# Kernel tuning notes

Measured on AMD Instinct MI355X. Metric: run time of the kernel, lower is better.

The kernel has to match this reference:

```python
import jax, jax.numpy as jnp
import numpy as np

DIM = 2048
NUM_HEADS = 16
NUM_KV_HEADS = 4
HEAD_DIM = DIM // NUM_HEADS  # 128
GROUP = NUM_HEADS // NUM_KV_HEADS  # queries per kv head
B, N = 2, 2048


def setup_inputs() -> dict:
    key = jax.random.key(0)
    ks = jax.random.split(key, 5)
    s = 1.0 / np.sqrt(DIM)
    return {
        "x": jax.random.normal(ks[0], (B, N, DIM), dtype=jnp.float32),
        "Wq": jax.random.normal(ks[1], (DIM, DIM), dtype=jnp.float32) * s,
        "Wk": jax.random.normal(ks[2], (DIM, NUM_KV_HEADS * HEAD_DIM), dtype=jnp.float32) * s,
        "Wv": jax.random.normal(ks[3], (DIM, NUM_KV_HEADS * HEAD_DIM), dtype=jnp.float32) * s,
        "Wo": jax.random.normal(ks[4], (DIM, DIM), dtype=jnp.float32) * s,
    }


def reference(x, Wq, Wk, Wv, Wo):
    Bc, Nc, C = x.shape
    scale = HEAD_DIM ** -0.5
    # projections -> [B, H, N, D] / [B, Hkv, N, D]
    q = (x @ Wq).reshape(Bc, Nc, NUM_HEADS, HEAD_DIM).transpose(0, 2, 1, 3)
    k = (x @ Wk).reshape(Bc, Nc, NUM_KV_HEADS, HEAD_DIM).transpose(0, 2, 1, 3)
    v = (x @ Wv).reshape(Bc, Nc, NUM_KV_HEADS, HEAD_DIM).transpose(0, 2, 1, 3)
    # repeat_interleave over head dim: kv head i serves query heads [i*G, (i+1)*G)
    k = jnp.repeat(k, GROUP, axis=1)  # [B, H, N, D]
    v = jnp.repeat(v, GROUP, axis=1)
    attn = jnp.einsum("bhqd,bhkd->bhqk", q, k) * scale
    attn = jax.nn.softmax(attn, axis=-1)
    out = jnp.einsum("bhqk,bhkd->bhqd", attn, v)  # [B, H, N, D]
    out = out.transpose(0, 2, 1, 3).reshape(Bc, Nc, C)
    return out @ Wo
```

## Files before the change

### kernel.cpp

```cpp
#include <hip/hip_runtime.h>
#include <hip/hip_bf16.h>
#include <cstdint>
#include <cstddef>

typedef __bf16 bf16;
typedef __attribute__((ext_vector_type(8))) __bf16 bf16x8;
typedef __attribute__((ext_vector_type(4))) float f32x4;
typedef __attribute__((ext_vector_type(16))) float f32x16;
typedef unsigned int u32;
typedef __attribute__((ext_vector_type(2))) unsigned int u32x2;

#define DEVINL __device__ __forceinline__

#define QPRESCALE 0.12751741530470082f

DEVINL void gload16(const void* g, void* l) {
  __builtin_amdgcn_global_load_lds(
      (const __attribute__((address_space(1))) void*)g,
      (__attribute__((address_space(3))) void*)l, 16, 0, 0);
}

DEVINL f32x4 mfma16(bf16x8 a, bf16x8 b, f32x4 c) {
  return __builtin_amdgcn_mfma_f32_16x16x32_bf16(a, b, c, 0, 0, 0);
}
DEVINL f32x16 mfma32(bf16x8 a, bf16x8 b, f32x16 c) {
  return __builtin_amdgcn_mfma_f32_32x32x16_bf16(a, b, c, 0, 0, 0);
}
DEVINL u32 cvtpk(float lo, float hi) {
  u32 r;
  asm("v_cvt_pk_bf16_f32 %0, %1, %2" : "=v"(r) : "v"(lo), "v"(hi));
  return r;
}
DEVINL void plswap(u32& a, u32& b) {
  asm("v_permlane32_swap_b32 %0, %1" : "+v"(a), "+v"(b));
}

__global__ __launch_bounds__(256) void prep_kernel(const float* __restrict__ x,
                                                   const float* __restrict__ Wq,
                                                   const float* __restrict__ Wk,
                                                   const float* __restrict__ Wv,
                                                   const float* __restrict__ Wo,
                                                   bf16* __restrict__ xbf,
                                                   bf16* __restrict__ WqkvT,
                                                   bf16* __restrict__ WoT) {
  const int bid = blockIdx.x, t = threadIdx.x;
  if (bid < 4096) {
    int i = bid * 256 + t;
    f32x4 a = ((const f32x4*)x)[2 * i];
    f32x4 b2 = ((const f32x4*)x)[2 * i + 1];
    bf16x8 v;
#pragma unroll
    for (int k = 0; k < 4; ++k) { v[k] = (bf16)a[k]; v[4 + k] = (bf16)b2[k]; }
    ((bf16x8*)xbf)[i] = v;
    return;
  }
  __shared__ float tile[64][65];
  const float* src;
  bf16* dst;
  int N, blk;
  if (bid < 5120)      { src = Wq; dst = WqkvT;                        N = 2048; blk = bid - 4096; }
  else if (bid < 5376) { src = Wk; dst = WqkvT + (size_t)2048 * 2048;  N = 512;  blk = bid - 5120; }
  else if (bid < 5632) { src = Wv; dst = WqkvT + (size_t)2560 * 2048;  N = 512;  blk = bid - 5376; }
  else                 { src = Wo; dst = WoT;                          N = 2048; blk = bid - 5632; }
  const int K = 2048;
  int nt = N >> 6;
  int n0 = (blk % nt) << 6;
  int k0 = (blk / nt) << 6;
  int c = t & 63, rb = t >> 6;
#pragma unroll
  for (int rr = 0; rr < 16; ++rr) {
    int row = rr * 4 + rb;
    tile[row][c] = src[(size_t)(k0 + row) * N + n0 + c];
  }
  __syncthreads();
#pragma unroll
  for (int rr = 0; rr < 16; ++rr) {
    int nrow = rr * 4 + rb;
    dst[(size_t)(n0 + nrow) * K + k0 + c] = (bf16)tile[c][nrow];
  }
}

template <int EPI>
__global__ __launch_bounds__(256) void gemm_bt_kernel(const bf16* __restrict__ A,
                                                      const bf16* __restrict__ BT,
                                                      float* __restrict__ Cout,
                                                      int Mtiles,
                                                      bf16* __restrict__ qb,
                                                      bf16* __restrict__ kb_,
                                                      bf16* __restrict__ vtb) {
  __shared__ __align__(16) unsigned char smem[32768];
  const int t = threadIdx.x, w = t >> 6, lane = t & 63;
  const int l4 = lane >> 4, l16 = lane & 15;
  const int bm = blockIdx.x % Mtiles, bn = blockIdx.x / Mtiles;
  const int wm = w >> 1, wn = w & 1;

  const char* aP[2];
  const char* bP[2];
#pragma unroll
  for (int p = 0; p < 2; ++p) {
    int g = p * 256 + t;
    aP[p] = (const char*)A + (size_t)(bm * 128 + (g >> 2)) * 4096 + (g & 3) * 16;
    bP[p] = (const char*)BT + (size_t)(bn * 128 + (g >> 2)) * 4096 + (g & 3) * 16;
  }
  const unsigned ldsW = w * 1024;

  auto STAGE = [&](unsigned buf, int k0) {
    gload16(aP[0] + k0, smem + buf * 16384 + ldsW);
    gload16(aP[1] + k0, smem + buf * 16384 + 4096 + ldsW);
    gload16(bP[0] + k0, smem + buf * 16384 + 8192 + ldsW);
    gload16(bP[1] + k0, smem + buf * 16384 + 12288 + ldsW);
  };

  const f32x4 fz = {0.f, 0.f, 0.f, 0.f};
  f32x4 acc[4][4];
#pragma unroll
  for (int i = 0; i < 4; ++i)
#pragma unroll
    for (int j = 0; j < 4; ++j) acc[i][j] = fz;

  const int arow = 64 * wm + l16, brow = 64 * wn + l16, kbyte = 16 * l4;

  STAGE(0, 0);
  __syncthreads();

#pragma unroll 2
  for (int tt = 0; tt < 64; ++tt) {
    const unsigned buf = tt & 1;
    if (tt < 63) STAGE(buf ^ 1u, (tt + 1) * 64);
    bf16x8 af[4], bfr[4];
#pragma unroll
    for (int i = 0; i < 4; ++i)
      af[i] = *(const bf16x8*)(smem + buf * 16384 + (arow + 16 * i) * 64 + kbyte);
#pragma unroll
    for (int j = 0; j < 4; ++j)
      bfr[j] = *(const bf16x8*)(smem + buf * 16384 + 8192 + (brow + 16 * j) * 64 + kbyte);
#pragma unroll
    for (int i = 0; i < 4; ++i)
#pragma unroll
      for (int j = 0; j < 4; ++j)
        acc[i][j] = mfma16(af[i], bfr[j], acc[i][j]);
    __syncthreads();
  }

  const int r0 = bm * 128 + 64 * wm + 4 * l4;
  if (EPI == 1) {
#pragma unroll
    for (int j = 0; j < 4; ++j) {
      int col = bn * 128 + 64 * wn + 16 * j + l16;
#pragma unroll
      for (int i = 0; i < 4; ++i)
#pragma unroll
        for (int r = 0; r < 4; ++r)
          Cout[(size_t)(r0 + 16 * i + r) * 2048 + col] = acc[i][j][r];
    }
  } else {
    const int bq = bm >> 4;
#pragma unroll
    for (int j = 0; j < 4; ++j) {
      int col = bn * 128 + 64 * wn + 16 * j + l16;
      if (bn < 16) {
        int hh = col >> 7, d = col & 127;
        bf16* dst = qb + (size_t)((bq * 16 + hh) * 2048) * 128 + d;
#pragma unroll
        for (int i = 0; i < 4; ++i)
#pragma unroll
          for (int r = 0; r < 4; ++r) {
            int n = (r0 + 16 * i + r) & 2047;
            dst[(size_t)n * 128] = (bf16)(acc[i][j][r] * QPRESCALE);
          }
      } else if (bn < 20) {
        int kv = (col >> 7) - 16, d = col & 127;
        bf16* dst = kb_ + (size_t)((bq * 4 + kv) * 2048) * 128 + d;
#pragma unroll
        for (int i = 0; i < 4; ++i)
#pragma unroll
          for (int r = 0; r < 4; ++r) {
            int n = (r0 + 16 * i + r) & 2047;
            dst[(size_t)n * 128] = (bf16)acc[i][j][r];
          }
      } else {
        int kv = (col >> 7) - 20, d = col & 127;
        bf16* dst = vtb + ((size_t)(bq * 4 + kv) * 128 + d) * 2048;
#pragma unroll
        for (int i = 0; i < 4; ++i)
#pragma unroll
          for (int r = 0; r < 4; ++r) {
            int n = (r0 + 16 * i + r) & 2047;
            dst[n] = (bf16)acc[i][j][r];
          }
      }
    }
  }
}

__global__ __launch_bounds__(256, 2) void attn_kernel(const bf16* __restrict__ Q,
                                                      const bf16* __restrict__ K,
                                                      const bf16* __restrict__ VT,
                                                      bf16* __restrict__ AO) {
  __shared__ __align__(16) unsigned char smem[65536];
  const int t = threadIdx.x, w = t >> 6, lane = t & 63;
  const int q = lane & 31, hi = lane >> 5;
  const int pair = blockIdx.x >> 4;
  const int q00 = (blockIdx.x & 15) * 128 + w * 32;
  const int b = pair >> 4, h = pair & 15, kvh = h >> 2;

  bf16x8 qf[8];
  {
    const char* qbase = (const char*)Q +
        ((size_t)((b * 16 + h) * 2048 + q00 + q) * 128 + 8 * hi) * 2;
#pragma unroll
    for (int dk = 0; dk < 8; ++dk) qf[dk] = *(const bf16x8*)(qbase + dk * 32);
  }

  f32x16 acc[4];
#pragma unroll
  for (int dt = 0; dt < 4; ++dt)
#pragma unroll
    for (int r = 0; r < 16; ++r) acc[dt][r] = 0.0f;
  float lacc[16];
#pragma unroll
  for (int r = 0; r < 16; ++r) lacc[r] = 0.0f;

  const char* Kg = (const char*)K + (size_t)((b * 4 + kvh) * 2048) * 256;
  const char* Vg = (const char*)VT + (size_t)((b * 4 + kvh) * 128) * 4096;

  auto STAGE_K = [&](int itn) {
    const unsigned base = (unsigned)(itn & 1) * 16384u;
    const int kb = itn * 64;
#pragma unroll
    for (int p = 0; p < 4; ++p) {
      int g = p * 256 + t;
      int row = g >> 4, cb = (g & 15) * 16;
      gload16(Kg + (size_t)(kb + row) * 256 + (cb ^ ((row & 15) << 4)),
              smem + base + p * 4096 + w * 1024);
    }
  };
  auto STAGE_V = [&](int itn) {
    const unsigned base = 32768u + (unsigned)(itn & 1) * 16384u;
    const int kb = itn * 64;
#pragma unroll
    for (int p = 0; p < 4; ++p) {
      int g = p * 256 + t;
      int row = g >> 3, cb = (g & 7) * 16;
      gload16(Vg + (size_t)row * 4096 + kb * 2 + (cb ^ ((row & 7) << 4)),
              smem + base + p * 4096 + w * 1024);
    }
  };

  auto SMFMA = [&](int itn, f32x16& s0, f32x16& s1) {
    const unsigned base = (unsigned)(itn & 1) * 16384u;
    const unsigned swq = (q & 15) << 4;
#pragma unroll
    for (int r = 0; r < 16; ++r) { s0[r] = 0.0f; s1[r] = 0.0f; }
    __builtin_amdgcn_s_setprio(1);
#pragma unroll
    for (int dk = 0; dk < 8; ++dk) {
      const int cb = dk * 32 + 16 * hi;
      bf16x8 k0 = *(const bf16x8*)(smem + base + q * 256 + (cb ^ swq));
      bf16x8 k1 = *(const bf16x8*)(smem + base + (q + 32) * 256 + (cb ^ swq));
      s0 = mfma32(k0, qf[dk], s0);
      s1 = mfma32(k1, qf[dk], s1);
    }
    __builtin_amdgcn_s_setprio(0);
  };

  auto SOFTMAX = [&](f32x16& s0, f32x16& s1, bf16x8* pa) {
    float p0[16], p1[16];
#pragma unroll
    for (int r = 0; r < 16; ++r) {
      p0[r] = __builtin_amdgcn_exp2f(s0[r]);
      p1[r] = __builtin_amdgcn_exp2f(s1[r]);
    }
#pragma unroll
    for (int r = 0; r < 16; ++r) lacc[r] += p0[r] + p1[r];
#pragma unroll
    for (int ks = 0; ks < 4; ++ks) {
      const int bs = (ks & 1) * 8;
      float* P = (ks >> 1) ? p1 : p0;
      u32 A0 = cvtpk(P[bs + 0], P[bs + 1]);
      u32 A1 = cvtpk(P[bs + 2], P[bs + 3]);
      u32 B0 = cvtpk(P[bs + 4], P[bs + 5]);
      u32 B1 = cvtpk(P[bs + 6], P[bs + 7]);
      plswap(A0, B0);
      plswap(A1, B1);
      union { u32 u[4]; bf16x8 v; } pu;
      pu.u[0] = A0; pu.u[1] = A1; pu.u[2] = B0; pu.u[3] = B1;
      pa[ks] = pu.v;
    }
  };

  auto FUSED = [&](int itn, f32x16& sP0, f32x16& sP1, f32x16& sN0, f32x16& sN1) {
    bf16x8 pa[4];
    SOFTMAX(sP0, sP1, pa);
    const unsigned kbase = (unsigned)(itn & 1) * 16384u;
    const unsigned vbase = 32768u + (unsigned)((itn - 1) & 1) * 16384u;
    const unsigned swq = (q & 15) << 4;
    const unsigned swd = (q & 7) << 4;
#pragma unroll
    for (int r = 0; r < 16; ++r) { sN0[r] = 0.0f; sN1[r] = 0.0f; }
    __builtin_amdgcn_s_setprio(1);
#pragma unroll
    for (int step = 0; step < 8; ++step) {
      const int cb = step * 32 + 16 * hi;
      bf16x8 k0 = *(const bf16x8*)(smem + kbase + q * 256 + (cb ^ swq));
      bf16x8 k1 = *(const bf16x8*)(smem + kbase + (q + 32) * 256 + (cb ^ swq));
      const int ks = step >> 1, dt0 = (step & 1) * 2, dt1 = dt0 + 1;
      const int kcol = ks * 32 + 16 * hi;
      bf16x8 va0 = *(const bf16x8*)(smem + vbase + (dt0 * 32 + q) * 128 + (kcol ^ swd));
      bf16x8 va1 = *(const bf16x8*)(smem + vbase + (dt1 * 32 + q) * 128 + (kcol ^ swd));
      sN0 = mfma32(k0, qf[step], sN0);
      acc[dt0] = mfma32(va0, pa[ks], acc[dt0]);
      sN1 = mfma32(k1, qf[step], sN1);
      acc[dt1] = mfma32(va1, pa[ks], acc[dt1]);
    }
    __builtin_amdgcn_s_setprio(0);
  };

  auto FINLAST = [&](int itn, f32x16& sP0, f32x16& sP1) {
    bf16x8 pa[4];
    SOFTMAX(sP0, sP1, pa);
    const unsigned vbase = 32768u + (unsigned)(itn & 1) * 16384u;
    const unsigned swd = (q & 7) << 4;
    __builtin_amdgcn_s_setprio(1);
#pragma unroll
    for (int ks = 0; ks < 4; ++ks) {
      const int kcol = ks * 32 + 16 * hi;
      bf16x8 va0 = *(const bf16x8*)(smem + vbase + (0 * 32 + q) * 128 + (kcol ^ swd));
      bf16x8 va1 = *(const bf16x8*)(smem + vbase + (1 * 32 + q) * 128 + (kcol ^ swd));
      bf16x8 va2 = *(const bf16x8*)(smem + vbase + (2 * 32 + q) * 128 + (kcol ^ swd));
      bf16x8 va3 = *(const bf16x8*)(smem + vbase + (3 * 32 + q) * 128 + (kcol ^ swd));
      acc[0] = mfma32(va0, pa[ks], acc[0]);
      acc[1] = mfma32(va1, pa[ks], acc[1]);
      acc[2] = mfma32(va2, pa[ks], acc[2]);
      acc[3] = mfma32(va3, pa[ks], acc[3]);
    }
    __builtin_amdgcn_s_setprio(0);
  };

  f32x16 sA0, sA1, sB0, sB1;
  STAGE_K(0);
  __syncthreads();

  STAGE_K(1);
  STAGE_V(0);
  SMFMA(0, sA0, sA1);
  __syncthreads();

#pragma unroll 1
  for (int i = 1; i < 31; i += 2) {
    STAGE_K(i + 1);
    STAGE_V(i);
    FUSED(i, sA0, sA1, sB0, sB1);
    __syncthreads();
    STAGE_K(i + 2);
    STAGE_V(i + 1);
    FUSED(i + 1, sB0, sB1, sA0, sA1);
    __syncthreads();
  }

  STAGE_V(31);
  FUSED(31, sA0, sA1, sB0, sB1);
  __syncthreads();
  FINLAST(31, sB0, sB1);

  float tl[16];
#pragma unroll
  for (int r = 0; r < 16; ++r) tl[r] = lacc[r];
#pragma unroll
  for (int st = 8; st; st >>= 1)
#pragma unroll
    for (int r = 0; r < 8; ++r)
      if (r < st) tl[r] += tl[r + st];
  float l0 = tl[0];
  l0 += __shfl_xor(l0, 32, 64);
  const float inv = 1.0f / l0;
  bf16* aorow = AO + (size_t)(b * 2048 + q00 + q) * 2048 + h * 128;
#pragma unroll
  for (int dt = 0; dt < 4; ++dt)
#pragma unroll
    for (int rq = 0; rq < 4; ++rq) {
      u32 w0 = cvtpk(acc[dt][rq * 4 + 0] * inv, acc[dt][rq * 4 + 1] * inv);
      u32 w1 = cvtpk(acc[dt][rq * 4 + 2] * inv, acc[dt][rq * 4 + 3] * inv);
      u32x2 pr; pr.x = w0; pr.y = w1;
      *(u32x2*)(aorow + dt * 32 + rq * 8 + 4 * hi) = pr;
    }
}

extern "C" void kernel_launch(void* const* d_in, const int* in_sizes, int n_in,
                              void* d_out, int out_size, void* d_ws, size_t ws_size,
                              hipStream_t stream) {
  const float* x = (const float*)d_in[0];
  const float* Wq = (const float*)d_in[1];
  const float* Wk = (const float*)d_in[2];
  const float* Wv = (const float*)d_in[3];
  const float* Wo = (const float*)d_in[4];

  char* ws = (char*)d_ws;
  bf16* xbf = (bf16*)(ws);
  bf16* WqkvT = (bf16*)(ws + 16777216);
  bf16* WoT = (bf16*)(ws + 29360128);
  bf16* Qbuf = (bf16*)(ws + 37748736);
  bf16* Kbuf = (bf16*)(ws + 54525952);
  bf16* VTbuf = (bf16*)(ws + 58720256);

  prep_kernel<<<6656, 256, 0, stream>>>(x, Wq, Wk, Wv, Wo, xbf, WqkvT, WoT);
  gemm_bt_kernel<0><<<768, 256, 0, stream>>>(xbf, WqkvT, nullptr, 32, Qbuf, Kbuf, VTbuf);
  attn_kernel<<<512, 256, 0, stream>>>(Qbuf, Kbuf, VTbuf, xbf);
  gemm_bt_kernel<1><<<512, 256, 0, stream>>>(xbf, WoT, (float*)d_out, 32, nullptr, nullptr, nullptr);
}
```

Baseline: 195.0 us.

## Process 64 query rows per wave in attention to reuse K/V fragments

Each wave now handles two 32-row query tiles instead of one, so every K and V fragment read from LDS feeds two MFMAs. The attention grid is halved to 256 blocks and launch bounds drop to one block per CU. This cuts LDS read traffic and K/V global staging per query. In exchange it roughly doubles register pressure (accumulators, scores, Q fragments) and lowers occupancy. With 256 blocks on a 256-CU part, each CU may get only one block, leaving little latency hiding.

```diff
diff --git a/kernel.cpp b/kernel.cpp
--- a/kernel.cpp
+++ b/kernel.cpp
@@ -193,33 +193,36 @@
   }
 }
 
-__global__ __launch_bounds__(256, 2) void attn_kernel(const bf16* __restrict__ Q,
+__global__ __launch_bounds__(256, 1) void attn_kernel(const bf16* __restrict__ Q,
                                                       const bf16* __restrict__ K,
                                                       const bf16* __restrict__ VT,
                                                       bf16* __restrict__ AO) {
   __shared__ __align__(16) unsigned char smem[65536];
   const int t = threadIdx.x, w = t >> 6, lane = t & 63;
   const int q = lane & 31, hi = lane >> 5;
-  const int pair = blockIdx.x >> 4;
-  const int q00 = (blockIdx.x & 15) * 128 + w * 32;
+  const int pair = blockIdx.x >> 3;
+  const int q00 = (blockIdx.x & 7) * 256 + w * 64;
   const int b = pair >> 4, h = pair & 15, kvh = h >> 2;
 
-  bf16x8 qf[8];
+  bf16x8 qf0[8], qf1[8];
   {
     const char* qbase = (const char*)Q +
         ((size_t)((b * 16 + h) * 2048 + q00 + q) * 128 + 8 * hi) * 2;
 #pragma unroll
-    for (int dk = 0; dk < 8; ++dk) qf[dk] = *(const bf16x8*)(qbase + dk * 32);
-  }
-
-  f32x16 acc[4];
+    for (int dk = 0; dk < 8; ++dk) {
+      qf0[dk] = *(const bf16x8*)(qbase + dk * 32);
+      qf1[dk] = *(const bf16x8*)(qbase + 32 * 256 + dk * 32);
+    }
+  }
+
+  f32x16 acc0[4], acc1[4];
 #pragma unroll
   for (int dt = 0; dt < 4; ++dt)
 #pragma unroll
-    for (int r = 0; r < 16; ++r) acc[dt][r] = 0.0f;
-  float lacc[16];
-#pragma unroll
-  for (int r = 0; r < 16; ++r) lacc[r] = 0.0f;
+    for (int r = 0; r < 16; ++r) { acc0[dt][r] = 0.0f; acc1[dt][r] = 0.0f; }
+  float lacc0[16], lacc1[16];
+#pragma unroll
+  for (int r = 0; r < 16; ++r) { lacc0[r] = 0.0f; lacc1[r] = 0.0f; }
 
   const char* Kg = (const char*)K + (size_t)((b * 4 + kvh) * 2048) * 256;
   const char* Vg = (const char*)VT + (size_t)((b * 4 + kvh) * 128) * 4096;
@@ -247,24 +250,26 @@
     }
   };
 
-  auto SMFMA = [&](int itn, f32x16& s0, f32x16& s1) {
+  auto SMFMA = [&](int itn, f32x16& s00, f32x16& s01, f32x16& s10, f32x16& s11) {
     const unsigned base = (unsigned)(itn & 1) * 16384u;
     const unsigned swq = (q & 15) << 4;
 #pragma unroll
-    for (int r = 0; r < 16; ++r) { s0[r] = 0.0f; s1[r] = 0.0f; }
+    for (int r = 0; r < 16; ++r) { s00[r] = 0.0f; s01[r] = 0.0f; s10[r] = 0.0f; s11[r] = 0.0f; }
     __builtin_amdgcn_s_setprio(1);
 #pragma unroll
     for (int dk = 0; dk < 8; ++dk) {
       const int cb = dk * 32 + 16 * hi;
       bf16x8 k0 = *(const bf16x8*)(smem + base + q * 256 + (cb ^ swq));
       bf16x8 k1 = *(const bf16x8*)(smem + base + (q + 32) * 256 + (cb ^ swq));
-      s0 = mfma32(k0, qf[dk], s0);
-      s1 = mfma32(k1, qf[dk], s1);
+      s00 = mfma32(k0, qf0[dk], s00);
+      s10 = mfma32(k0, qf1[dk], s10);
+      s01 = mfma32(k1, qf0[dk], s01);
+      s11 = mfma32(k1, qf1[dk], s11);
     }
     __builtin_amdgcn_s_setprio(0);
   };
 
-  auto SOFTMAX = [&](f32x16& s0, f32x16& s1, bf16x8* pa) {
+  auto SOFTMAX = [&](f32x16& s0, f32x16& s1, bf16x8* pa, float (&lac)[16]) {
     float p0[16], p1[16];
 #pragma unroll
     for (int r = 0; r < 16; ++r) {
@@ -272,7 +277,7 @@
       p1[r] = __builtin_amdgcn_exp2f(s1[r]);
     }
 #pragma unroll
-    for (int r = 0; r < 16; ++r) lacc[r] += p0[r] + p1[r];
+    for (int r = 0; r < 16; ++r) lac[r] += p0[r] + p1[r];
 #pragma unroll
     for (int ks = 0; ks < 4; ++ks) {
       const int bs = (ks & 1) * 8;
@@ -289,15 +294,18 @@
     }
   };
 
-  auto FUSED = [&](int itn, f32x16& sP0, f32x16& sP1, f32x16& sN0, f32x16& sN1) {
-    bf16x8 pa[4];
-    SOFTMAX(sP0, sP1, pa);
+  auto FUSED = [&](int itn,
+                   f32x16& sP00, f32x16& sP01, f32x16& sP10, f32x16& sP11,
+                   f32x16& sN00, f32x16& sN01, f32x16& sN10, f32x16& sN11) {
+    bf16x8 pa0[4], pa1[4];
+    SOFTMAX(sP00, sP01, pa0, lacc0);
+    SOFTMAX(sP10, sP11, pa1, lacc1);
     const unsigned kbase = (unsigned)(itn & 1) * 16384u;
     const unsigned vbase = 32768u + (unsigned)((itn - 1) & 1) * 16384u;
     const unsigned swq = (q & 15) << 4;
     const unsigned swd = (q & 7) << 4;
 #pragma unroll
-    for (int r = 0; r < 16; ++r) { sN0[r] = 0.0f; sN1[r] = 0.0f; }
+    for (int r = 0; r < 16; ++r) { sN00[r] = 0.0f; sN01[r] = 0.0f; sN10[r] = 0.0f; sN11[r] = 0.0f; }
     __builtin_amdgcn_s_setprio(1);
 #pragma unroll
     for (int step = 0; step < 8; ++step) {
@@ -308,82 +316,110 @@
       const int kcol = ks * 32 + 16 * hi;
       bf16x8 va0 = *(const bf16x8*)(smem + vbase + (dt0 * 32 + q) * 128 + (kcol ^ swd));
       bf16x8 va1 = *(const bf16x8*)(smem + vbase + (dt1 * 32 + q) * 128 + (kcol ^ swd));
-      sN0 = mfma32(k0, qf[step], sN0);
-      acc[dt0] = mfma32(va0, pa[ks], acc[dt0]);
-      sN1 = mfma32(k1, qf[step], sN1);
-      acc[dt1] = mfma32(va1, pa[ks], acc[dt1]);
+      sN00 = mfma32(k0, qf0[step], sN00);
+      acc0[dt0] = mfma32(va0, pa0[ks], acc0[dt0]);
+      sN10 = mfma32(k0, qf1[step], sN10);
+      acc1[dt0] = mfma32(va0, pa1[ks], acc1[dt0]);
+      sN01 = mfma32(k1, qf0[step], sN01);
+      acc0[dt1] = mfma32(va1, pa0[ks], acc0[dt1]);
+      sN11 = mfma32(k1, qf1[step], sN11);
+      acc1[dt1] = mfma32(va1, pa1[ks], acc1[dt1]);
     }
     __builtin_amdgcn_s_setprio(0);
   };
 
-  auto FINLAST = [&](int itn, f32x16& sP0, f32x16& sP1) {
-    bf16x8 pa[4];
-    SOFTMAX(sP0, sP1, pa);
+  auto FINLAST = [&](int itn, f32x16& sP00, f32x16& sP01, f32x16& sP10, f32x16& sP11) {
+    bf16x8 pa0[4], pa1[4];
+    SOFTMAX(sP00, sP01, pa0, lacc0);
+    SOFTMAX(sP10, sP11, pa1, lacc1);
     const unsigned vbase = 32768u + (unsigned)(itn & 1) * 16384u;
     const unsigned swd = (q & 7) << 4;
     __builtin_amdgcn_s_setprio(1);
 #pragma unroll
     for (int ks = 0; ks < 4; ++ks) {
       const int kcol = ks * 32 + 16 * hi;
-      bf16x8 va0 = *(const bf16x8*)(smem + vbase + (0 * 32 + q) * 128 + (kcol ^ swd));
-      bf16x8 va1 = *(const bf16x8*)(smem + vbase + (1 * 32 + q) * 128 + (kcol ^ swd));
-      bf16x8 va2 = *(const bf16x8*)(smem + vbase + (2 * 32 + q) * 128 + (kcol ^ swd));
-      bf16x8 va3 = *(const bf16x8*)(smem + vbase + (3 * 32 + q) * 128 + (kcol ^ swd));
-      acc[0] = mfma32(va0, pa[ks], acc[0]);
-      acc[1] = mfma32(va1, pa[ks], acc[1]);
-      acc[2] = mfma32(va2, pa[ks], acc[2]);
-      acc[3] = mfma32(va3, pa[ks], acc[3]);
+#pragma unroll
+      for (int dt = 0; dt < 4; ++dt) {
+        bf16x8 va = *(const bf16x8*)(smem + vbase + (dt * 32 + q) * 128 + (kcol ^ swd));
+        acc0[dt] = mfma32(va, pa0[ks], acc0[dt]);
+        acc1[dt] = mfma32(va, pa1[ks], acc1[dt]);
+      }
     }
     __builtin_amdgcn_s_setprio(0);
   };
 
-  f32x16 sA0, sA1, sB0, sB1;
+  f32x16 sA00, sA01, sA10, sA11, sB00, sB01, sB10, sB11;
   STAGE_K(0);
   __syncthreads();
 
   STAGE_K(1);
   STAGE_V(0);
-  SMFMA(0, sA0, sA1);
+  SMFMA(0, sA00, sA01, sA10, sA11);
   __syncthreads();
 
 #pragma unroll 1
   for (int i = 1; i < 31; i += 2) {
     STAGE_K(i + 1);
     STAGE_V(i);
-    FUSED(i, sA0, sA1, sB0, sB1);
+    FUSED(i, sA00, sA01, sA10, sA11, sB00, sB01, sB10, sB11);
     __syncthreads();
     STAGE_K(i + 2);
     STAGE_V(i + 1);
-    FUSED(i + 1, sB0, sB1, sA0, sA1);
+    FUSED(i + 1, sB00, sB01, sB10, sB11, sA00, sA01, sA10, sA11);
     __syncthreads();
   }
 
   STAGE_V(31);
-  FUSED(31, sA0, sA1, sB0, sB1);
+  FUSED(31, sA00, sA01, sA10, sA11, sB00, sB01, sB10, sB11);
   __syncthreads();
-  FINLAST(31, sB0, sB1);
-
-  float tl[16];
-#pragma unroll
-  for (int r = 0; r < 16; ++r) tl[r] = lacc[r];
-#pragma unroll
-  for (int st = 8; st; st >>= 1)
-#pragma unroll
-    for (int r = 0; r < 8; ++r)
-      if (r < st) tl[r] += tl[r + st];
-  float l0 = tl[0];
-  l0 += __shfl_xor(l0, 32, 64);
-  const float inv = 1.0f / l0;
-  bf16* aorow = AO + (size_t)(b * 2048 + q00 + q) * 2048 + h * 128;
-#pragma unroll
-  for (int dt = 0; dt < 4; ++dt)
-#pragma unroll
-    for (int rq = 0; rq < 4; ++rq) {
-      u32 w0 = cvtpk(acc[dt][rq * 4 + 0] * inv, acc[dt][rq * 4 + 1] * inv);
-      u32 w1 = cvtpk(acc[dt][rq * 4 + 2] * inv, acc[dt][rq * 4 + 3] * inv);
-      u32x2 pr; pr.x = w0; pr.y = w1;
-      *(u32x2*)(aorow + dt * 32 + rq * 8 + 4 * hi) = pr;
-    }
+  FINLAST(31, sB00, sB01, sB10, sB11);
+
+  {
+    float tl[16];
+#pragma unroll
+    for (int r = 0; r < 16; ++r) tl[r] = lacc0[r];
+#pragma unroll
+    for (int st = 8; st; st >>= 1)
+#pragma unroll
+      for (int r = 0; r < 8; ++r)
+        if (r < st) tl[r] += tl[r + st];
+    float l0 = tl[0];
+    l0 += __shfl_xor(l0, 32, 64);
+    const float inv = 1.0f / l0;
+    bf16* aorow = AO + (size_t)(b * 2048 + q00 + q) * 2048 + h * 128;
+#pragma unroll
+    for (int dt = 0; dt < 4; ++dt)
+#pragma unroll
+      for (int rq = 0; rq < 4; ++rq) {
+        u32 w0 = cvtpk(acc0[dt][rq * 4 + 0] * inv, acc0[dt][rq * 4 + 1] * inv);
+        u32 w1 = cvtpk(acc0[dt][rq * 4 + 2] * inv, acc0[dt][rq * 4 + 3] * inv);
+        u32x2 pr; pr.x = w0; pr.y = w1;
+        *(u32x2*)(aorow + dt * 32 + rq * 8 + 4 * hi) = pr;
+      }
+  }
+  {
+    float tl[16];
+#pragma unroll
+    for (int r = 0; r < 16; ++r) tl[r] = lacc1[r];
+#pragma unroll
+    for (int st = 8; st; st >>= 1)
+#pragma unroll
+      for (int r = 0; r < 8; ++r)
+        if (r < st) tl[r] += tl[r + st];
+    float l1 = tl[0];
+    l1 += __shfl_xor(l1, 32, 64);
+    const float inv = 1.0f / l1;
+    bf16* aorow = AO + (size_t)(b * 2048 + q00 + 32 + q) * 2048 + h * 128;
+#pragma unroll
+    for (int dt = 0; dt < 4; ++dt)
+#pragma unroll
+      for (int rq = 0; rq < 4; ++rq) {
+        u32 w0 = cvtpk(acc1[dt][rq * 4 + 0] * inv, acc1[dt][rq * 4 + 1] * inv);
+        u32 w1 = cvtpk(acc1[dt][rq * 4 + 2] * inv, acc1[dt][rq * 4 + 3] * inv);
+        u32x2 pr; pr.x = w0; pr.y = w1;
+        *(u32x2*)(aorow + dt * 32 + rq * 8 + 4 * hi) = pr;
+      }
+  }
 }
 
 extern "C" void kernel_launch(void* const* d_in, const int* in_sizes, int n_in,
@@ -405,6 +441,6 @@
 
   prep_kernel<<<6656, 256, 0, stream>>>(x, Wq, Wk, Wv, Wo, xbf, WqkvT, WoT);
   gemm_bt_kernel<0><<<768, 256, 0, stream>>>(xbf, WqkvT, nullptr, 32, Qbuf, Kbuf, VTbuf);
-  attn_kernel<<<512, 256, 0, stream>>>(Qbuf, Kbuf, VTbuf, xbf);
+  attn_kernel<<<256, 256, 0, stream>>>(Qbuf, Kbuf, VTbuf, xbf);
   gemm_bt_kernel<1><<<512, 256, 0, stream>>>(xbf, WoT, (float*)d_out, 32, nullptr, nullptr, nullptr);
 }
```

After: 195.4 us. No clear change (+0.2%).
